# Kernel tuning notes

Hardware: AMD Instinct MI355X
Metric: run time of the kernel (lower is better)

## Reference

```python
import jax, jax.numpy as jnp
import numpy as np

E, H, D = 512, 8, 64          # embed_dim, num_heads, head_dim
MAX_SUM = 128                  # max_summary (embedding table has MAX_SUM+1 rows, row 0 = padding)
SCALE = D ** -0.5


def _linear(x, w, b):
    y = jnp.einsum('...i,oi->...o', x, w)
    return y if b is None else y + b


def setup_inputs() -> dict:
    key = jax.random.key(0)
    ks = jax.random.split(key, 16)
    R, B, S = 2048, 2, 128

    def xav(k, shape, gain=1.0):
        fan_in, fan_out = shape[1], shape[0]
        a = gain * np.sqrt(6.0 / (fan_in + fan_out))
        return jax.random.uniform(k, shape, jnp.float32, -a, a)

    g = 1.0 / np.sqrt(2.0)
    embed_table = jax.random.normal(ks[0], (MAX_SUM + 1, E), jnp.float32) * 0.02
    embed_table = embed_table.at[0].set(0.0)  # padding_idx=0
    return {
        'reg_x': jax.random.normal(ks[1], (R, B, E), jnp.float32),
        'sum_token_ids': jax.random.randint(ks[2], (B, S), 0, MAX_SUM),
        'sum_len': S,
        'reg_len': R,
        'embed_table': embed_table,
        'wq1': xav(ks[3], (E, E), g), 'bq1': jnp.zeros((E,), jnp.float32),
        'wq2': xav(ks[4], (E, E), g), 'bq2': jnp.zeros((E,), jnp.float32),
        'wk': xav(ks[5], (E, E), g),  'bk': jnp.zeros((E,), jnp.float32),
        'wv': xav(ks[6], (E, E), g),  'bv': jnp.zeros((E,), jnp.float32),
        'wo': xav(ks[7], (E, E)),     'bo': jnp.zeros((E,), jnp.float32),
        'sum_gate_w': xav(ks[8], (E, E)),
        'reg_gate_w': xav(ks[9], (E, E)),
        'gate_bias': jax.random.normal(ks[10], (E,), jnp.float32),
    }


def reference(reg_x, sum_token_ids, sum_len, reg_len, embed_table,
              wq1, bq1, wq2, bq2, wk, bk, wv, bv, wo, bo,
              sum_gate_w, reg_gate_w, gate_bias):
    R, B, _ = reg_x.shape
    S = sum_token_ids.shape[1]

    # regular keys/values (shared across all stages)
    reg_k = _linear(reg_x, wk, bk).reshape(R, B, H, D)
    reg_v = _linear(reg_x, wv, bv).reshape(R, B, H, D)

    # ---- stage 1: summary queries (learned summary embeddings) attend to regular tokens
    sum_q = embed_table[sum_token_ids.T].reshape(S, B, H, D)  # [S,B,H,D]
    scores_sr = jnp.einsum('sbhd,rbhd->bhsr', sum_q * SCALE, reg_k)
    w_sr = jax.nn.softmax(scores_sr, axis=-1)
    sum_x2 = jnp.einsum('bhsr,rbhd->sbhd', w_sr, reg_v)       # summary K=V for stage 2

    # ---- stage 2: regular queries attend to summary tokens
    reg_q1 = _linear(reg_x, wq1, bq1).reshape(R, B, H, D)
    scores_rs = jnp.einsum('rbhd,sbhd->bhrs', reg_q1 * SCALE, sum_x2)
    w_rs = jax.nn.softmax(scores_rs, axis=-1)
    sum_output = jnp.einsum('bhrs,sbhd->rbhd', w_rs, sum_x2).reshape(R, B, E)

    # ---- stage 3: regular self-attention
    reg_q2 = _linear(reg_x, wq2, bq2).reshape(R, B, H, D)
    scores_rr = jnp.einsum('qbhd,kbhd->bhqk', reg_q2 * SCALE, reg_k)
    w_rr = jax.nn.softmax(scores_rr, axis=-1)
    reg_output = jnp.einsum('bhqk,kbhd->qbhd', w_rr, reg_v).reshape(R, B, E)

    # ---- gated fusion of summary path and regular path
    gate = jax.nn.sigmoid(_linear(sum_output, sum_gate_w, None)
                          + _linear(reg_output, reg_gate_w, None) + gate_bias)
    attn_output = gate * sum_output + (1.0 - gate) * reg_output
    return _linear(attn_output, wo, bo)
```

## Files before the change

kernel.cpp:

```cpp
#include <hip/hip_runtime.h>
#include <cstdint>
#include <cstddef>

constexpr int R_ = 2048;
constexpr int B_ = 2;
constexpr int S_ = 128;
constexpr int E_ = 512;
constexpr int H_ = 8;
constexpr int D_ = 64;
constexpr int N_ = R_ * B_;
constexpr float SCALE_ = 0.125f;

typedef short bf8_t __attribute__((ext_vector_type(8)));
typedef short bf4_t __attribute__((ext_vector_type(4)));
typedef float f32x4 __attribute__((ext_vector_type(4)));
typedef float f32x16 __attribute__((ext_vector_type(16)));

#define MFMA16(a, b, c) __builtin_amdgcn_mfma_f32_16x16x32_bf16((a), (b), (c), 0, 0, 0)
#define MFMA32(a, b, c) __builtin_amdgcn_mfma_f32_32x32x16_bf16((a), (b), (c), 0, 0, 0)

__device__ __forceinline__ unsigned short f2bf(float f) {
  unsigned u = __builtin_bit_cast(unsigned, f);
  unsigned r = u + 0x7FFFu + ((u >> 16) & 1u);
  return (unsigned short)(r >> 16);
}
__device__ __forceinline__ float bf2f(unsigned short h) {
  unsigned u = ((unsigned)h) << 16;
  return __builtin_bit_cast(float, u);
}

struct WSplitJob { const float* src; unsigned short* dst; };
struct WSplit7 { WSplitJob j[7]; };

__global__ __launch_bounds__(256)
void split_w7_kernel(WSplit7 P)
{
  const WSplitJob jb = P.j[blockIdx.y];
  const int idx = blockIdx.x * 256 + threadIdx.x;
  const int r = idx >> 9, c = idx & 511;
  const float v = jb.src[idx];
  const unsigned short hi = f2bf(v);
  const unsigned short lo = f2bf(v - bf2f(hi));
  unsigned short* d = jb.dst + (size_t)r * 1536 + c;
  d[0] = hi; d[512] = hi; d[1024] = lo;
}

__global__ __launch_bounds__(256)
void split_a_kernel(const float* __restrict__ src, unsigned short* __restrict__ dst)
{
  const int idx = blockIdx.x * 256 + threadIdx.x;
  const int r = idx >> 9, c = idx & 511;
  const float v = src[idx];
  const unsigned short hi = f2bf(v);
  unsigned short* d = dst + ((size_t)r << 10) + c;
  d[0] = hi; d[512] = f2bf(v - bf2f(hi));
}

__global__ __launch_bounds__(256)
void gather_split_kernel(const float* __restrict__ table, const int* __restrict__ ids,
                         unsigned short* __restrict__ qhi, unsigned short* __restrict__ qlo)
{
  const int idx = blockIdx.x * 256 + threadIdx.x;
  const int d = idx & 63;
  const int s = (idx >> 6) & 127;
  const int h = (idx >> 13) & 7;
  const int b = idx >> 16;
  const float v = table[(size_t)ids[b * S_ + s] * E_ + h * 64 + d] * SCALE_;
  const unsigned short hi = f2bf(v);
  qhi[idx] = hi;
  qlo[idx] = f2bf(v - bf2f(hi));
}

struct GemmOut {
  const unsigned short* W;
  const float* bias;
  float scale;
  float* Cf;
  unsigned short* hi;
  unsigned short* lo;
  int mode;
};
struct GemmOuts4 { GemmOut o[4]; };

__global__ __launch_bounds__(256, 4)
void gemm_split_kernel(const unsigned short* __restrict__ A, GemmOuts4 P)
{
  const GemmOut g = P.o[blockIdx.z];
  __shared__ unsigned short As[128][48];
  __shared__ unsigned short Ws[64][48];

  const int tid = threadIdx.x;
  const int w = tid >> 6;
  const int l = tid & 63;
  const int lr = l & 15;
  const int lg = l >> 4;
  const int n0 = blockIdx.x * 128;
  const int o0 = blockIdx.y * 64;

  f32x4 acc[2][4];
#pragma unroll
  for (int m = 0; m < 2; ++m)
#pragma unroll
    for (int n = 0; n < 4; ++n) acc[m][n] = (f32x4){0.f, 0.f, 0.f, 0.f};

  const int ar = tid >> 1;
  const int ac = (tid & 1) * 16;
  const int wr = tid >> 2;
  const int wc = (tid & 3) * 8;

  bf8_t ra0 = *(const bf8_t*)(A + (size_t)(n0 + ar) * 1024 + ac);
  bf8_t ra1 = *(const bf8_t*)(A + (size_t)(n0 + ar) * 1024 + ac + 8);
  bf8_t rw0 = *(const bf8_t*)(g.W + (size_t)(o0 + wr) * 1536 + wc);

  for (int k0 = 0; k0 < 1536; k0 += 32) {
    __syncthreads();
    *(bf8_t*)&As[ar][ac] = ra0;
    *(bf8_t*)&As[ar][ac + 8] = ra1;
    *(bf8_t*)&Ws[wr][wc] = rw0;
    __syncthreads();
    if (k0 + 32 < 1536) {
      const int ak = (k0 + 32) & 1023;
      ra0 = *(const bf8_t*)(A + (size_t)(n0 + ar) * 1024 + ak + ac);
      ra1 = *(const bf8_t*)(A + (size_t)(n0 + ar) * 1024 + ak + ac + 8);
      rw0 = *(const bf8_t*)(g.W + (size_t)(o0 + wr) * 1536 + k0 + 32 + wc);
    }

    bf8_t bvs[4];
#pragma unroll
    for (int n = 0; n < 4; ++n)
      bvs[n] = *(const bf8_t*)&Ws[n * 16 + lr][lg * 8];
#pragma unroll
    for (int m = 0; m < 2; ++m) {
      bf8_t av = *(const bf8_t*)&As[w * 32 + m * 16 + lr][lg * 8];
#pragma unroll
      for (int n = 0; n < 4; ++n)
        acc[m][n] = MFMA16(av, bvs[n], acc[m][n]);
    }
  }

#pragma unroll
  for (int m = 0; m < 2; ++m)
#pragma unroll
    for (int n = 0; n < 4; ++n)
#pragma unroll
      for (int r = 0; r < 4; ++r) {
        const int row = n0 + w * 32 + m * 16 + lg * 4 + r;
        const int col = o0 + n * 16 + lr;
        float v = acc[m][n][r];
        if (g.bias) v += g.bias[col];
        v *= g.scale;
        if (g.mode == 0) {
          g.Cf[((size_t)row << 9) + col] = v;
        } else {
          const int bb = row & 1, rr = row >> 1;
          const int hh = col >> 6, dd = col & 63;
          size_t id;
          if (g.mode == 1) id = (((size_t)(bb * H_ + hh) * R_) + rr) * 64 + dd;
          else             id = (((size_t)(bb * H_ + hh) * 64) + dd) * R_ + rr;
          const unsigned short hv = f2bf(v);
          g.hi[id] = hv;
          g.lo[id] = f2bf(v - bf2f(hv));
        }
      }
}

__global__ __launch_bounds__(256, 4)
void gate_blend_gemm_kernel(const unsigned short* __restrict__ A1,
                            const unsigned short* __restrict__ A2,
                            const unsigned short* __restrict__ W1,
                            const unsigned short* __restrict__ W2,
                            const float* __restrict__ gb,
                            unsigned short* __restrict__ attnP)
{
  __shared__ unsigned short As[128][48];
  __shared__ unsigned short Ws[64][48];

  const int tid = threadIdx.x;
  const int w = tid >> 6;
  const int l = tid & 63;
  const int lr = l & 15;
  const int lg = l >> 4;
  const int n0 = blockIdx.x * 128;
  const int o0 = blockIdx.y * 64;

  f32x4 acc[2][4];
#pragma unroll
  for (int m = 0; m < 2; ++m)
#pragma unroll
    for (int n = 0; n < 4; ++n) acc[m][n] = (f32x4){0.f, 0.f, 0.f, 0.f};

  const int ar = tid >> 1;
  const int ac = (tid & 1) * 16;
  const int wr = tid >> 2;
  const int wc = (tid & 3) * 8;

  auto aP = [&](int kk) {
    const unsigned short* Ax = (kk < 48) ? A1 : A2;
    const int k0 = ((kk < 48) ? kk : kk - 48) * 32;
    return Ax + (size_t)(n0 + ar) * 1024 + (k0 & 1023) + ac;
  };
  auto wP = [&](int kk) {
    const unsigned short* Wx = (kk < 48) ? W1 : W2;
    const int k0 = ((kk < 48) ? kk : kk - 48) * 32;
    return Wx + (size_t)(o0 + wr) * 1536 + k0 + wc;
  };

  bf8_t ra0 = *(const bf8_t*)aP(0);
  bf8_t ra1 = *(const bf8_t*)(aP(0) + 8);
  bf8_t rw0 = *(const bf8_t*)wP(0);

  for (int kk = 0; kk < 96; ++kk) {
    __syncthreads();
    *(bf8_t*)&As[ar][ac] = ra0;
    *(bf8_t*)&As[ar][ac + 8] = ra1;
    *(bf8_t*)&Ws[wr][wc] = rw0;
    __syncthreads();
    if (kk + 1 < 96) {
      ra0 = *(const bf8_t*)aP(kk + 1);
      ra1 = *(const bf8_t*)(aP(kk + 1) + 8);
      rw0 = *(const bf8_t*)wP(kk + 1);
    }

    bf8_t bvs[4];
#pragma unroll
    for (int n = 0; n < 4; ++n)
      bvs[n] = *(const bf8_t*)&Ws[n * 16 + lr][lg * 8];
#pragma unroll
    for (int m = 0; m < 2; ++m) {
      bf8_t av = *(const bf8_t*)&As[w * 32 + m * 16 + lr][lg * 8];
#pragma unroll
      for (int n = 0; n < 4; ++n)
        acc[m][n] = MFMA16(av, bvs[n], acc[m][n]);
    }
  }

#pragma unroll
  for (int m = 0; m < 2; ++m)
#pragma unroll
    for (int n = 0; n < 4; ++n)
#pragma unroll
      for (int r = 0; r < 4; ++r) {
        const int row = n0 + w * 32 + m * 16 + lg * 4 + r;
        const int col = o0 + n * 16 + lr;
        const float t = acc[m][n][r] + gb[col];
        const float gt = 1.0f / (1.0f + __expf(-t));
        const size_t base = (size_t)row << 10;
        const float so = bf2f(A1[base + col]) + bf2f(A1[base + 512 + col]);
        const float ro = bf2f(A2[base + col]) + bf2f(A2[base + 512 + col]);
        const float a = gt * so + (1.0f - gt) * ro;
        const unsigned short hv = f2bf(a);
        attnP[base + col] = hv;
        attnP[base + 512 + col] = f2bf(a - bf2f(hv));
      }
}

__global__ __launch_bounds__(256, 2)
void flash_partial_kernel(const unsigned short* __restrict__ Qhi, const unsigned short* __restrict__ Qlo,
                          const unsigned short* __restrict__ Khi, const unsigned short* __restrict__ Klo,
                          const unsigned short* __restrict__ VtHi, const unsigned short* __restrict__ VtLo,
                          int q_len, int kv_len, int chunk, int zsplit,
                          float* __restrict__ accA, float* __restrict__ accB,
                          float* __restrict__ mlP)
{
  __shared__ unsigned short KsH[32][72];
  __shared__ unsigned short KsL[32][72];
  __shared__ unsigned short VsH[64][40];
  __shared__ unsigned short VsL[64][40];

  const int tid = threadIdx.x;
  const int w = tid >> 6;
  const int l = tid & 63;
  const int lq = l & 31;
  const int hi = l >> 5;
  const int bh = blockIdx.y;
  const int q0 = blockIdx.x * 128;
  const int c = blockIdx.z;
  const int kvbeg = c * chunk;
  const int kvend = kvbeg + chunk;
  const int qrow = q0 + w * 32 + lq;

  bf8_t qh[4], ql[4];
  {
    const size_t qbase = ((size_t)bh * q_len + qrow) * 64;
#pragma unroll
    for (int kd = 0; kd < 4; ++kd) {
      qh[kd] = *(const bf8_t*)(Qhi + qbase + kd * 16 + hi * 8);
      ql[kd] = *(const bf8_t*)(Qlo + qbase + kd * 16 + hi * 8);
    }
  }

  f32x16 acc0 = {0,0,0,0,0,0,0,0,0,0,0,0,0,0,0,0};
  f32x16 acc1 = {0,0,0,0,0,0,0,0,0,0,0,0,0,0,0,0};
  float mrow = -INFINITY;
  float lrow = 0.0f;

  const int sr = tid >> 3;
  const int sc = (tid & 7) * 8;
  const int vd = tid >> 2;
  const int vc = (tid & 3) * 8;

  bf8_t rkh, rkl, rvh, rvl;
  {
    const size_t kb = ((size_t)bh * kv_len + kvbeg + sr) * 64 + sc;
    rkh = *(const bf8_t*)(Khi + kb);
    rkl = *(const bf8_t*)(Klo + kb);
    const size_t vb = ((size_t)bh * 64 + vd) * kv_len + kvbeg + vc;
    rvh = *(const bf8_t*)(VtHi + vb);
    rvl = *(const bf8_t*)(VtLo + vb);
  }

  for (int kv0 = kvbeg; kv0 < kvend; kv0 += 32) {
    __syncthreads();
    *(bf8_t*)&KsH[sr][sc] = rkh;
    *(bf8_t*)&KsL[sr][sc] = rkl;
    *(bf8_t*)&VsH[vd][vc] = rvh;
    *(bf8_t*)&VsL[vd][vc] = rvl;
    __syncthreads();
    if (kv0 + 32 < kvend) {
      const size_t kb = ((size_t)bh * kv_len + kv0 + 32 + sr) * 64 + sc;
      rkh = *(const bf8_t*)(Khi + kb);
      rkl = *(const bf8_t*)(Klo + kb);
      const size_t vb = ((size_t)bh * 64 + vd) * kv_len + kv0 + 32 + vc;
      rvh = *(const bf8_t*)(VtHi + vb);
      rvl = *(const bf8_t*)(VtLo + vb);
    }

    f32x16 s = {0,0,0,0,0,0,0,0,0,0,0,0,0,0,0,0};
#pragma unroll
    for (int kd = 0; kd < 4; ++kd) {
      const bf8_t kfh = *(const bf8_t*)&KsH[lq][kd * 16 + hi * 8];
      const bf8_t kfl = *(const bf8_t*)&KsL[lq][kd * 16 + hi * 8];
      s = MFMA32(kfh, qh[kd], s);
      s = MFMA32(kfh, ql[kd], s);
      s = MFMA32(kfl, qh[kd], s);
    }

    float mx = s[0];
#pragma unroll
    for (int r = 1; r < 16; ++r) mx = fmaxf(mx, s[r]);
    mx = fmaxf(mx, __shfl_xor(mx, 32));
    const float m2 = fmaxf(mrow, mx);
    const float f = __expf(mrow - m2);
    mrow = m2;
    float p[16];
    float ts = 0.f;
#pragma unroll
    for (int r = 0; r < 16; ++r) { p[r] = __expf(s[r] - m2); ts += p[r]; }
    ts += __shfl_xor(ts, 32);
    lrow = lrow * f + ts;
#pragma unroll
    for (int r = 0; r < 16; ++r) { acc0[r] *= f; acc1[r] *= f; }

    bf8_t pah[2], pal[2];
#pragma unroll
    for (int ks = 0; ks < 2; ++ks)
#pragma unroll
      for (int j = 0; j < 8; ++j) {
        const float v = p[ks * 8 + j];
        const unsigned u = __builtin_bit_cast(unsigned, v);
        pah[ks][j] = (short)(u >> 16);
        pal[ks][j] = (short)f2bf(v - __builtin_bit_cast(float, u & 0xFFFF0000u));
      }

#pragma unroll
    for (int ks = 0; ks < 2; ++ks) {
      {
        const bf4_t vh0 = *(const bf4_t*)&VsH[lq][ks * 16 + hi * 4];
        const bf4_t vh1 = *(const bf4_t*)&VsH[lq][ks * 16 + 8 + hi * 4];
        const bf4_t vl0 = *(const bf4_t*)&VsL[lq][ks * 16 + hi * 4];
        const bf4_t vl1 = *(const bf4_t*)&VsL[lq][ks * 16 + 8 + hi * 4];
        const bf8_t vfh = {vh0[0], vh0[1], vh0[2], vh0[3], vh1[0], vh1[1], vh1[2], vh1[3]};
        const bf8_t vfl = {vl0[0], vl0[1], vl0[2], vl0[3], vl1[0], vl1[1], vl1[2], vl1[3]};
        acc0 = MFMA32(vfh, pah[ks], acc0);
        acc0 = MFMA32(vfh, pal[ks], acc0);
        acc0 = MFMA32(vfl, pah[ks], acc0);
      }
      {
        const bf4_t vh0 = *(const bf4_t*)&VsH[32 + lq][ks * 16 + hi * 4];
        const bf4_t vh1 = *(const bf4_t*)&VsH[32 + lq][ks * 16 + 8 + hi * 4];
        const bf4_t vl0 = *(const bf4_t*)&VsL[32 + lq][ks * 16 + hi * 4];
        const bf4_t vl1 = *(const bf4_t*)&VsL[32 + lq][ks * 16 + 8 + hi * 4];
        const bf8_t vfh = {vh0[0], vh0[1], vh0[2], vh0[3], vh1[0], vh1[1], vh1[2], vh1[3]};
        const bf8_t vfl = {vl0[0], vl0[1], vl0[2], vl0[3], vl1[0], vl1[1], vl1[2], vl1[3]};
        acc1 = MFMA32(vfh, pah[ks], acc1);
        acc1 = MFMA32(vfh, pal[ks], acc1);
        acc1 = MFMA32(vfl, pah[ks], acc1);
      }
    }
  }

  const size_t cstride = (size_t)16 * q_len * 64;
  float* accbase = (c < zsplit) ? accA + (size_t)c * cstride
                                : accB + (size_t)(c - zsplit) * cstride;
  float* rowp = accbase + ((size_t)bh * q_len + qrow) * 64;
#pragma unroll
  for (int rg = 0; rg < 4; ++rg) {
    *(float4*)(rowp + rg * 8 + hi * 4) =
        make_float4(acc0[rg * 4 + 0], acc0[rg * 4 + 1], acc0[rg * 4 + 2], acc0[rg * 4 + 3]);
    *(float4*)(rowp + 32 + rg * 8 + hi * 4) =
        make_float4(acc1[rg * 4 + 0], acc1[rg * 4 + 1], acc1[rg * 4 + 2], acc1[rg * 4 + 3]);
  }
  if (l < 32) {
    const int q = q0 + w * 32 + l;
    *(float2*)&mlP[((size_t)(c * 16 + bh) * q_len + q) * 2] = make_float2(mrow, lrow);
  }
}

__global__ __launch_bounds__(256)
void merge_x2_kernel(const float* __restrict__ acc, const float* __restrict__ ml,
                     unsigned short* __restrict__ X2hi, unsigned short* __restrict__ X2lo,
                     unsigned short* __restrict__ X2Thi, unsigned short* __restrict__ X2Tlo)
{
  const int idx = blockIdx.x * 256 + threadIdx.x;
  const int d = idx & 63;
  const int q = (idx >> 6) & 127;
  const int bh = idx >> 13;
  float M = -INFINITY;
#pragma unroll
  for (int c = 0; c < 16; ++c)
    M = fmaxf(M, ml[((size_t)(c * 16 + bh) * 128 + q) * 2]);
  float ls = 0.f, o = 0.f;
#pragma unroll
  for (int c = 0; c < 16; ++c) {
    const size_t mi = ((size_t)(c * 16 + bh) * 128 + q) * 2;
    const float wgt = __expf(ml[mi] - M);
    ls += wgt * ml[mi + 1];
    o += wgt * acc[(size_t)c * 131072 + ((size_t)bh * 128 + q) * 64 + d];
  }
  const float v = o / ls;
  const unsigned short hv = f2bf(v);
  const unsigned short lv = f2bf(v - bf2f(hv));
  X2hi[((size_t)bh * 128 + q) * 64 + d] = hv;
  X2lo[((size_t)bh * 128 + q) * 64 + d] = lv;
  X2Thi[((size_t)bh * 64 + d) * 128 + q] = hv;
  X2Tlo[((size_t)bh * 64 + d) * 128 + q] = lv;
}

__global__ __launch_bounds__(256)
void merge_rows_kernel(const float* __restrict__ accA, const float* __restrict__ accB,
                       const float* __restrict__ ml, int q_len, int qbits, int nc,
                       unsigned short* __restrict__ OutP)
{
  const int idx = blockIdx.x * 256 + threadIdx.x;
  const int d = idx & 63;
  const int q = (idx >> 6) & (q_len - 1);
  const int bh = idx >> (6 + qbits);
  float M = -INFINITY;
  for (int c = 0; c < nc; ++c)
    M = fmaxf(M, ml[((size_t)(c * 16 + bh) * q_len + q) * 2]);
  float ls = 0.f, o = 0.f;
  const size_t aoff = ((size_t)bh * q_len + q) * 64 + d;
  for (int c = 0; c < nc; ++c) {
    const size_t mi = ((size_t)(c * 16 + bh) * q_len + q) * 2;
    const float wgt = __expf(ml[mi] - M);
    ls += wgt * ml[mi + 1];
    const float* a = (c == 0) ? accA : accB;
    o += wgt * a[aoff];
  }
  const float v = o / ls;
  const int b = bh >> 3, h = bh & 7;
  const size_t nrow = (size_t)q * B_ + b;
  const int col = h * 64 + d;
  const unsigned short hv = f2bf(v);
  OutP[nrow * 1024 + col] = hv;
  OutP[nrow * 1024 + 512 + col] = f2bf(v - bf2f(hv));
}

extern "C" void kernel_launch(void* const* d_in, const int* in_sizes, int n_in,
                              void* d_out, int out_size, void* d_ws, size_t ws_size,
                              hipStream_t stream)
{
  const float* reg_x = (const float*)d_in[0];
  const int*   ids   = (const int*)d_in[1];
  const float* table = (const float*)d_in[4];
  const float* wq1 = (const float*)d_in[5];  const float* bq1 = (const float*)d_in[6];
  const float* wq2 = (const float*)d_in[7];  const float* bq2 = (const float*)d_in[8];
  const float* wk  = (const float*)d_in[9];  const float* bk  = (const float*)d_in[10];
  const float* wv  = (const float*)d_in[11]; const float* bv  = (const float*)d_in[12];
  const float* wo  = (const float*)d_in[13]; const float* bo  = (const float*)d_in[14];
  const float* sgw = (const float*)d_in[15];
  const float* rgw = (const float*)d_in[16];
  const float* gb  = (const float*)d_in[17];
  float* out = (float*)d_out;
  char* W = (char*)d_ws;

  const size_t WSLOT  = 1572864;
  const size_t oApair = 0;
  const size_t oW     = 8388608;
  const size_t oKhi   = oW + 7 * WSLOT;
  const size_t oKlo   = oKhi + 4194304;
  const size_t oVtHi  = oKlo + 4194304;
  const size_t oVtLo  = oVtHi + 4194304;
  const size_t oQ1hi  = oVtLo + 4194304;
  const size_t oQ1lo  = oQ1hi + 4194304;
  const size_t oQ2hi  = oQ1lo + 4194304;
  const size_t oQ2lo  = oQ2hi + 4194304;
  const size_t oAcc1  = oQ2lo + 4194304;
  const size_t oSQhi  = oAcc1 + 8388608;
  const size_t oSQlo  = oSQhi + 262144;
  const size_t oX2hi  = oSQlo + 262144;
  const size_t oX2lo  = oX2hi + 262144;
  const size_t oX2Thi = oX2lo + 262144;
  const size_t oX2Tlo = oX2Thi + 262144;
  const size_t oMl    = oX2Tlo + 262144;

  auto U16 = [&](size_t off) { return (unsigned short*)(W + off); };
  auto F32 = [&](size_t off) { return (float*)(W + off); };
  unsigned short* Apair  = U16(oApair);
  unsigned short* Wk3    = U16(oW + 0 * WSLOT);
  unsigned short* Wv3    = U16(oW + 1 * WSLOT);
  unsigned short* Wq13   = U16(oW + 2 * WSLOT);
  unsigned short* Wq23   = U16(oW + 3 * WSLOT);
  unsigned short* Wsg3   = U16(oW + 4 * WSLOT);
  unsigned short* Wrg3   = U16(oW + 5 * WSLOT);
  unsigned short* Wo3    = U16(oW + 6 * WSLOT);
  float*          accS   = F32(oApair);
  float*          accB3  = F32(oAcc1);
  float*          mlP    = F32(oMl);
  unsigned short* sout_p = U16(oQ1hi);
  unsigned short* rout_p = U16(oQ2hi);
  unsigned short* attn_p = U16(oKhi);

  const dim3 blk(256);

  split_a_kernel<<<8192, blk, 0, stream>>>(reg_x, Apair);
  WSplit7 ws7;
  ws7.j[0] = WSplitJob{wk,  Wk3};
  ws7.j[1] = WSplitJob{wv,  Wv3};
  ws7.j[2] = WSplitJob{wq1, Wq13};
  ws7.j[3] = WSplitJob{wq2, Wq23};
  ws7.j[4] = WSplitJob{sgw, Wsg3};
  ws7.j[5] = WSplitJob{rgw, Wrg3};
  ws7.j[6] = WSplitJob{wo,  Wo3};
  split_w7_kernel<<<dim3(1024, 7), blk, 0, stream>>>(ws7);
  gather_split_kernel<<<512, blk, 0, stream>>>(table, ids, U16(oSQhi), U16(oSQlo));

  GemmOuts4 proj;
  proj.o[0].W = Wk3;  proj.o[0].bias = bk;  proj.o[0].scale = 1.0f;   proj.o[0].Cf = nullptr;
  proj.o[0].hi = U16(oKhi);  proj.o[0].lo = U16(oKlo);  proj.o[0].mode = 1;
  proj.o[1].W = Wv3;  proj.o[1].bias = bv;  proj.o[1].scale = 1.0f;   proj.o[1].Cf = nullptr;
  proj.o[1].hi = U16(oVtHi); proj.o[1].lo = U16(oVtLo); proj.o[1].mode = 2;
  proj.o[2].W = Wq13; proj.o[2].bias = bq1; proj.o[2].scale = SCALE_; proj.o[2].Cf = nullptr;
  proj.o[2].hi = U16(oQ1hi); proj.o[2].lo = U16(oQ1lo); proj.o[2].mode = 1;
  proj.o[3].W = Wq23; proj.o[3].bias = bq2; proj.o[3].scale = SCALE_; proj.o[3].Cf = nullptr;
  proj.o[3].hi = U16(oQ2hi); proj.o[3].lo = U16(oQ2lo); proj.o[3].mode = 1;
  gemm_split_kernel<<<dim3(32, 8, 4), blk, 0, stream>>>(Apair, proj);

  flash_partial_kernel<<<dim3(1, 16, 16), blk, 0, stream>>>(
      U16(oSQhi), U16(oSQlo), U16(oKhi), U16(oKlo), U16(oVtHi), U16(oVtLo),
      S_, R_, 128, 16, accS, accS, mlP);
  merge_x2_kernel<<<512, blk, 0, stream>>>(accS, mlP,
      U16(oX2hi), U16(oX2lo), U16(oX2Thi), U16(oX2Tlo));

  flash_partial_kernel<<<dim3(16, 16, 1), blk, 0, stream>>>(
      U16(oQ1hi), U16(oQ1lo), U16(oX2hi), U16(oX2lo), U16(oX2Thi), U16(oX2Tlo),
      R_, S_, 128, 1, accS, accS, mlP);
  merge_rows_kernel<<<8192, blk, 0, stream>>>(accS, accS, mlP, R_, 11, 1, sout_p);

  flash_partial_kernel<<<dim3(16, 16, 2), blk, 0, stream>>>(
      U16(oQ2hi), U16(oQ2lo), U16(oKhi), U16(oKlo), U16(oVtHi), U16(oVtLo),
      R_, R_, 1024, 1, accS, accB3, mlP);
  merge_rows_kernel<<<8192, blk, 0, stream>>>(accS, accB3, mlP, R_, 11, 2, rout_p);

  gate_blend_gemm_kernel<<<dim3(32, 8), blk, 0, stream>>>(
      sout_p, rout_p, Wsg3, Wrg3, gb, attn_p);

  GemmOuts4 gf;
  gf.o[0].W = Wo3; gf.o[0].bias = bo; gf.o[0].scale = 1.0f; gf.o[0].Cf = out;
  gf.o[0].hi = nullptr; gf.o[0].lo = nullptr; gf.o[0].mode = 0;
  gf.o[1] = gf.o[0]; gf.o[2] = gf.o[0]; gf.o[3] = gf.o[0];
  gemm_split_kernel<<<dim3(32, 8, 1), blk, 0, stream>>>(attn_p, gf);
}
```

Before: 244.6 us.

## Fuse split kernels, widen flash KV tile, use exp2 with lazy rescale

```diff
diff --git a/kernel.cpp b/kernel.cpp
--- a/kernel.cpp
+++ b/kernel.cpp
@@ -10,11 +10,13 @@
 constexpr int D_ = 64;
 constexpr int N_ = R_ * B_;
 constexpr float SCALE_ = 0.125f;
+constexpr float LOG2E_ = 1.44269504088896340736f;
+constexpr float SLOG2E_ = SCALE_ * LOG2E_;
 
 typedef short bf8_t __attribute__((ext_vector_type(8)));
-typedef short bf4_t __attribute__((ext_vector_type(4)));
 typedef float f32x4 __attribute__((ext_vector_type(4)));
 typedef float f32x16 __attribute__((ext_vector_type(16)));
+typedef unsigned u32x4 __attribute__((ext_vector_type(4)));
 
 #define MFMA16(a, b, c) __builtin_amdgcn_mfma_f32_16x16x32_bf16((a), (b), (c), 0, 0, 0)
 #define MFMA32(a, b, c) __builtin_amdgcn_mfma_f32_32x32x16_bf16((a), (b), (c), 0, 0, 0)
@@ -28,47 +30,49 @@
   unsigned u = ((unsigned)h) << 16;
   return __builtin_bit_cast(float, u);
 }
+__device__ __forceinline__ int kvperm(int kv) {
+  return (kv & ~15) | (kv & 3) | ((kv & 4) << 1) | ((kv & 8) >> 1);
+}
 
 struct WSplitJob { const float* src; unsigned short* dst; };
 struct WSplit7 { WSplitJob j[7]; };
 
 __global__ __launch_bounds__(256)
-void split_w7_kernel(WSplit7 P)
+void fused_split_kernel(const float* __restrict__ reg_x, unsigned short* __restrict__ Apair,
+                        WSplit7 P, const float* __restrict__ table,
+                        const int* __restrict__ ids,
+                        unsigned short* __restrict__ sqhi, unsigned short* __restrict__ sqlo)
 {
-  const WSplitJob jb = P.j[blockIdx.y];
-  const int idx = blockIdx.x * 256 + threadIdx.x;
-  const int r = idx >> 9, c = idx & 511;
-  const float v = jb.src[idx];
-  const unsigned short hi = f2bf(v);
-  const unsigned short lo = f2bf(v - bf2f(hi));
-  unsigned short* d = jb.dst + (size_t)r * 1536 + c;
-  d[0] = hi; d[512] = hi; d[1024] = lo;
-}
-
-__global__ __launch_bounds__(256)
-void split_a_kernel(const float* __restrict__ src, unsigned short* __restrict__ dst)
-{
-  const int idx = blockIdx.x * 256 + threadIdx.x;
-  const int r = idx >> 9, c = idx & 511;
-  const float v = src[idx];
-  const unsigned short hi = f2bf(v);
-  unsigned short* d = dst + ((size_t)r << 10) + c;
-  d[0] = hi; d[512] = f2bf(v - bf2f(hi));
-}
-
-__global__ __launch_bounds__(256)
-void gather_split_kernel(const float* __restrict__ table, const int* __restrict__ ids,
-                         unsigned short* __restrict__ qhi, unsigned short* __restrict__ qlo)
-{
-  const int idx = blockIdx.x * 256 + threadIdx.x;
-  const int d = idx & 63;
-  const int s = (idx >> 6) & 127;
-  const int h = (idx >> 13) & 7;
-  const int b = idx >> 16;
-  const float v = table[(size_t)ids[b * S_ + s] * E_ + h * 64 + d] * SCALE_;
-  const unsigned short hi = f2bf(v);
-  qhi[idx] = hi;
-  qlo[idx] = f2bf(v - bf2f(hi));
+  const int bx = blockIdx.x;
+  const int tid = threadIdx.x;
+  if (bx < 8192) {
+    const int idx = bx * 256 + tid;
+    const int r = idx >> 9, c = idx & 511;
+    const float v = reg_x[idx];
+    const unsigned short hi = f2bf(v);
+    unsigned short* d = Apair + ((size_t)r << 10) + c;
+    d[0] = hi; d[512] = f2bf(v - bf2f(hi));
+  } else if (bx < 15360) {
+    const int bj = bx - 8192;
+    const WSplitJob jb = P.j[bj >> 10];
+    const int idx = (bj & 1023) * 256 + tid;
+    const int r = idx >> 9, c = idx & 511;
+    const float v = jb.src[idx];
+    const unsigned short hi = f2bf(v);
+    const unsigned short lo = f2bf(v - bf2f(hi));
+    unsigned short* d = jb.dst + (size_t)r * 1536 + c;
+    d[0] = hi; d[512] = hi; d[1024] = lo;
+  } else {
+    const int idx = (bx - 15360) * 256 + tid;
+    const int d = idx & 63;
+    const int s = (idx >> 6) & 127;
+    const int h = (idx >> 13) & 7;
+    const int b = idx >> 16;
+    const float v = table[(size_t)ids[b * S_ + s] * E_ + h * 64 + d] * SLOG2E_;
+    const unsigned short hi = f2bf(v);
+    sqhi[idx] = hi;
+    sqlo[idx] = f2bf(v - bf2f(hi));
+  }
 }
 
 struct GemmOut {
@@ -156,7 +160,7 @@
           const int hh = col >> 6, dd = col & 63;
           size_t id;
           if (g.mode == 1) id = (((size_t)(bb * H_ + hh) * R_) + rr) * 64 + dd;
-          else             id = (((size_t)(bb * H_ + hh) * 64) + dd) * R_ + rr;
+          else             id = (((size_t)(bb * H_ + hh) * 64) + dd) * R_ + kvperm(rr);
           const unsigned short hv = f2bf(v);
           g.hi[id] = hv;
           g.lo[id] = f2bf(v - bf2f(hv));
@@ -258,14 +262,14 @@
 void flash_partial_kernel(const unsigned short* __restrict__ Qhi, const unsigned short* __restrict__ Qlo,
                           const unsigned short* __restrict__ Khi, const unsigned short* __restrict__ Klo,
                           const unsigned short* __restrict__ VtHi, const unsigned short* __restrict__ VtLo,
-                          int q_len, int kv_len, int chunk, int zsplit,
+                          int q_len, int kv_len, int chunk, int zsplit, int out_mode,
                           float* __restrict__ accA, float* __restrict__ accB,
-                          float* __restrict__ mlP)
+                          float* __restrict__ mlP, unsigned short* __restrict__ OutP)
 {
-  __shared__ unsigned short KsH[32][72];
-  __shared__ unsigned short KsL[32][72];
-  __shared__ unsigned short VsH[64][40];
-  __shared__ unsigned short VsL[64][40];
+  __shared__ unsigned short KsH[64][72];
+  __shared__ unsigned short KsL[64][72];
+  __shared__ unsigned short VsH[64][72];
+  __shared__ unsigned short VsL[64][72];
 
   const int tid = threadIdx.x;
   const int w = tid >> 6;
@@ -294,115 +298,156 @@
   float mrow = -INFINITY;
   float lrow = 0.0f;
 
-  const int sr = tid >> 3;
-  const int sc = (tid & 7) * 8;
-  const int vd = tid >> 2;
-  const int vc = (tid & 3) * 8;
-
-  bf8_t rkh, rkl, rvh, rvl;
+  const int sr = tid >> 2;
+  const int sc = (tid & 3) * 16;
+
+  bf8_t rkh[2], rkl[2], rvh[2], rvl[2];
   {
     const size_t kb = ((size_t)bh * kv_len + kvbeg + sr) * 64 + sc;
-    rkh = *(const bf8_t*)(Khi + kb);
-    rkl = *(const bf8_t*)(Klo + kb);
-    const size_t vb = ((size_t)bh * 64 + vd) * kv_len + kvbeg + vc;
-    rvh = *(const bf8_t*)(VtHi + vb);
-    rvl = *(const bf8_t*)(VtLo + vb);
-  }
-
-  for (int kv0 = kvbeg; kv0 < kvend; kv0 += 32) {
+    rkh[0] = *(const bf8_t*)(Khi + kb);  rkh[1] = *(const bf8_t*)(Khi + kb + 8);
+    rkl[0] = *(const bf8_t*)(Klo + kb);  rkl[1] = *(const bf8_t*)(Klo + kb + 8);
+    const size_t vb = ((size_t)bh * 64 + sr) * kv_len + kvbeg + sc;
+    rvh[0] = *(const bf8_t*)(VtHi + vb); rvh[1] = *(const bf8_t*)(VtHi + vb + 8);
+    rvl[0] = *(const bf8_t*)(VtLo + vb); rvl[1] = *(const bf8_t*)(VtLo + vb + 8);
+  }
+
+  for (int kv0 = kvbeg; kv0 < kvend; kv0 += 64) {
     __syncthreads();
-    *(bf8_t*)&KsH[sr][sc] = rkh;
-    *(bf8_t*)&KsL[sr][sc] = rkl;
-    *(bf8_t*)&VsH[vd][vc] = rvh;
-    *(bf8_t*)&VsL[vd][vc] = rvl;
+    *(bf8_t*)&KsH[sr][sc] = rkh[0];  *(bf8_t*)&KsH[sr][sc + 8] = rkh[1];
+    *(bf8_t*)&KsL[sr][sc] = rkl[0];  *(bf8_t*)&KsL[sr][sc + 8] = rkl[1];
+    *(bf8_t*)&VsH[sr][sc] = rvh[0];  *(bf8_t*)&VsH[sr][sc + 8] = rvh[1];
+    *(bf8_t*)&VsL[sr][sc] = rvl[0];  *(bf8_t*)&VsL[sr][sc + 8] = rvl[1];
     __syncthreads();
-    if (kv0 + 32 < kvend) {
-      const size_t kb = ((size_t)bh * kv_len + kv0 + 32 + sr) * 64 + sc;
-      rkh = *(const bf8_t*)(Khi + kb);
-      rkl = *(const bf8_t*)(Klo + kb);
-      const size_t vb = ((size_t)bh * 64 + vd) * kv_len + kv0 + 32 + vc;
-      rvh = *(const bf8_t*)(VtHi + vb);
-      rvl = *(const bf8_t*)(VtLo + vb);
-    }
-
-    f32x16 s = {0,0,0,0,0,0,0,0,0,0,0,0,0,0,0,0};
+    if (kv0 + 64 < kvend) {
+      const size_t kb = ((size_t)bh * kv_len + kv0 + 64 + sr) * 64 + sc;
+      rkh[0] = *(const bf8_t*)(Khi + kb);  rkh[1] = *(const bf8_t*)(Khi + kb + 8);
+      rkl[0] = *(const bf8_t*)(Klo + kb);  rkl[1] = *(const bf8_t*)(Klo + kb + 8);
+      const size_t vb = ((size_t)bh * 64 + sr) * kv_len + kv0 + 64 + sc;
+      rvh[0] = *(const bf8_t*)(VtHi + vb); rvh[1] = *(const bf8_t*)(VtHi + vb + 8);
+      rvl[0] = *(const bf8_t*)(VtLo + vb); rvl[1] = *(const bf8_t*)(VtLo + vb + 8);
+    }
+
+    f32x16 s0 = {0,0,0,0,0,0,0,0,0,0,0,0,0,0,0,0};
+    f32x16 s1 = {0,0,0,0,0,0,0,0,0,0,0,0,0,0,0,0};
+    __builtin_amdgcn_s_setprio(1);
 #pragma unroll
     for (int kd = 0; kd < 4; ++kd) {
-      const bf8_t kfh = *(const bf8_t*)&KsH[lq][kd * 16 + hi * 8];
-      const bf8_t kfl = *(const bf8_t*)&KsL[lq][kd * 16 + hi * 8];
-      s = MFMA32(kfh, qh[kd], s);
-      s = MFMA32(kfh, ql[kd], s);
-      s = MFMA32(kfl, qh[kd], s);
-    }
-
-    float mx = s[0];
-#pragma unroll
-    for (int r = 1; r < 16; ++r) mx = fmaxf(mx, s[r]);
+      const bf8_t kfh0 = *(const bf8_t*)&KsH[lq][kd * 16 + hi * 8];
+      const bf8_t kfl0 = *(const bf8_t*)&KsL[lq][kd * 16 + hi * 8];
+      s0 = MFMA32(kfh0, qh[kd], s0);
+      s0 = MFMA32(kfh0, ql[kd], s0);
+      s0 = MFMA32(kfl0, qh[kd], s0);
+      const bf8_t kfh1 = *(const bf8_t*)&KsH[32 + lq][kd * 16 + hi * 8];
+      const bf8_t kfl1 = *(const bf8_t*)&KsL[32 + lq][kd * 16 + hi * 8];
+      s1 = MFMA32(kfh1, qh[kd], s1);
+      s1 = MFMA32(kfh1, ql[kd], s1);
+      s1 = MFMA32(kfl1, qh[kd], s1);
+    }
+    __builtin_amdgcn_s_setprio(0);
+
+    float mx = fmaxf(s0[0], s1[0]);
+#pragma unroll
+    for (int r = 1; r < 16; ++r) mx = fmaxf(mx, fmaxf(s0[r], s1[r]));
     mx = fmaxf(mx, __shfl_xor(mx, 32));
-    const float m2 = fmaxf(mrow, mx);
-    const float f = __expf(mrow - m2);
-    mrow = m2;
-    float p[16];
+    if (mx > mrow + 8.0f) {
+      const float f = exp2f(mrow - mx);
+      mrow = mx;
+      lrow *= f;
+#pragma unroll
+      for (int r = 0; r < 16; ++r) { acc0[r] *= f; acc1[r] *= f; }
+    }
     float ts = 0.f;
 #pragma unroll
-    for (int r = 0; r < 16; ++r) { p[r] = __expf(s[r] - m2); ts += p[r]; }
+    for (int r = 0; r < 16; ++r) { s0[r] = exp2f(s0[r] - mrow); ts += s0[r]; }
+#pragma unroll
+    for (int r = 0; r < 16; ++r) { s1[r] = exp2f(s1[r] - mrow); ts += s1[r]; }
     ts += __shfl_xor(ts, 32);
-    lrow = lrow * f + ts;
-#pragma unroll
-    for (int r = 0; r < 16; ++r) { acc0[r] *= f; acc1[r] *= f; }
-
-    bf8_t pah[2], pal[2];
-#pragma unroll
-    for (int ks = 0; ks < 2; ++ks)
-#pragma unroll
-      for (int j = 0; j < 8; ++j) {
-        const float v = p[ks * 8 + j];
-        const unsigned u = __builtin_bit_cast(unsigned, v);
-        pah[ks][j] = (short)(u >> 16);
-        pal[ks][j] = (short)f2bf(v - __builtin_bit_cast(float, u & 0xFFFF0000u));
+    lrow += ts;
+
+    bf8_t pah[4], pal[4];
+#pragma unroll
+    for (int n = 0; n < 2; ++n)
+#pragma unroll
+      for (int ks = 0; ks < 2; ++ks) {
+        u32x4 hp, lp;
+#pragma unroll
+        for (int p2 = 0; p2 < 4; ++p2) {
+          const float a = n ? s1[ks * 8 + p2 * 2]     : s0[ks * 8 + p2 * 2];
+          const float b = n ? s1[ks * 8 + p2 * 2 + 1] : s0[ks * 8 + p2 * 2 + 1];
+          const unsigned ua = __builtin_bit_cast(unsigned, a);
+          const unsigned ub = __builtin_bit_cast(unsigned, b);
+          hp[p2] = (ua >> 16) | (ub & 0xFFFF0000u);
+          const float la = a - __builtin_bit_cast(float, ua & 0xFFFF0000u);
+          const float lb = b - __builtin_bit_cast(float, ub & 0xFFFF0000u);
+          lp[p2] = (__builtin_bit_cast(unsigned, la) >> 16) |
+                   (__builtin_bit_cast(unsigned, lb) & 0xFFFF0000u);
+        }
+        pah[n * 2 + ks] = __builtin_bit_cast(bf8_t, hp);
+        pal[n * 2 + ks] = __builtin_bit_cast(bf8_t, lp);
       }
 
-#pragma unroll
-    for (int ks = 0; ks < 2; ++ks) {
-      {
-        const bf4_t vh0 = *(const bf4_t*)&VsH[lq][ks * 16 + hi * 4];
-        const bf4_t vh1 = *(const bf4_t*)&VsH[lq][ks * 16 + 8 + hi * 4];
-        const bf4_t vl0 = *(const bf4_t*)&VsL[lq][ks * 16 + hi * 4];
-        const bf4_t vl1 = *(const bf4_t*)&VsL[lq][ks * 16 + 8 + hi * 4];
-        const bf8_t vfh = {vh0[0], vh0[1], vh0[2], vh0[3], vh1[0], vh1[1], vh1[2], vh1[3]};
-        const bf8_t vfl = {vl0[0], vl0[1], vl0[2], vl0[3], vl1[0], vl1[1], vl1[2], vl1[3]};
-        acc0 = MFMA32(vfh, pah[ks], acc0);
-        acc0 = MFMA32(vfh, pal[ks], acc0);
-        acc0 = MFMA32(vfl, pah[ks], acc0);
+    __builtin_amdgcn_s_setprio(1);
+#pragma unroll
+    for (int n = 0; n < 2; ++n)
+#pragma unroll
+      for (int ks = 0; ks < 2; ++ks) {
+        const int vcol = n * 32 + ks * 16 + hi * 8;
+        const bf8_t ph = pah[n * 2 + ks];
+        const bf8_t pl = pal[n * 2 + ks];
+        {
+          const bf8_t vfh = *(const bf8_t*)&VsH[lq][vcol];
+          const bf8_t vfl = *(const bf8_t*)&VsL[lq][vcol];
+          acc0 = MFMA32(vfh, ph, acc0);
+          acc0 = MFMA32(vfh, pl, acc0);
+          acc0 = MFMA32(vfl, ph, acc0);
+        }
+        {
+          const bf8_t vfh = *(const bf8_t*)&VsH[32 + lq][vcol];
+          const bf8_t vfl = *(const bf8_t*)&VsL[32 + lq][vcol];
+          acc1 = MFMA32(vfh, ph, acc1);
+          acc1 = MFMA32(vfh, pl, acc1);
+          acc1 = MFMA32(vfl, ph, acc1);
+        }
       }
-      {
-        const bf4_t vh0 = *(const bf4_t*)&VsH[32 + lq][ks * 16 + hi * 4];
-        const bf4_t vh1 = *(const bf4_t*)&VsH[32 + lq][ks * 16 + 8 + hi * 4];
-        const bf4_t vl0 = *(const bf4_t*)&VsL[32 + lq][ks * 16 + hi * 4];
-        const bf4_t vl1 = *(const bf4_t*)&VsL[32 + lq][ks * 16 + 8 + hi * 4];
-        const bf8_t vfh = {vh0[0], vh0[1], vh0[2], vh0[3], vh1[0], vh1[1], vh1[2], vh1[3]};
-        const bf8_t vfl = {vl0[0], vl0[1], vl0[2], vl0[3], vl1[0], vl1[1], vl1[2], vl1[3]};
-        acc1 = MFMA32(vfh, pah[ks], acc1);
-        acc1 = MFMA32(vfh, pal[ks], acc1);
-        acc1 = MFMA32(vfl, pah[ks], acc1);
+    __builtin_amdgcn_s_setprio(0);
+  }
+
+  if (out_mode == 0) {
+    const size_t cstride = (size_t)16 * q_len * 64;
+    float* accbase = (c < zsplit) ? accA + (size_t)c * cstride
+                                  : accB + (size_t)(c - zsplit) * cstride;
+    float* rowp = accbase + ((size_t)bh * q_len + qrow) * 64;
+#pragma unroll
+    for (int rg = 0; rg < 4; ++rg) {
+      *(float4*)(rowp + rg * 8 + hi * 4) =
+          make_float4(acc0[rg * 4 + 0], acc0[rg * 4 + 1], acc0[rg * 4 + 2], acc0[rg * 4 + 3]);
+      *(float4*)(rowp + 32 + rg * 8 + hi * 4) =
+          make_float4(acc1[rg * 4 + 0], acc1[rg * 4 + 1], acc1[rg * 4 + 2], acc1[rg * 4 + 3]);
+    }
+    if (l < 32) {
+      const int q = q0 + w * 32 + l;
+      *(float2*)&mlP[((size_t)(c * 16 + bh) * q_len + q) * 2] = make_float2(mrow, lrow);
+    }
+  } else {
+    const float inv = 1.0f / lrow;
+    const int b = bh >> 3, h = bh & 7;
+    const size_t base = ((size_t)qrow * B_ + b) << 10;
+#pragma unroll
+    for (int hd = 0; hd < 2; ++hd)
+#pragma unroll
+      for (int rg = 0; rg < 4; ++rg) {
+        const int col = h * 64 + hd * 32 + rg * 8 + hi * 4;
+        ushort4 hv4, lv4;
+#pragma unroll
+        for (int i = 0; i < 4; ++i) {
+          const float v = (hd ? acc1[rg * 4 + i] : acc0[rg * 4 + i]) * inv;
+          const unsigned short hv = f2bf(v);
+          ((unsigned short*)&hv4)[i] = hv;
+          ((unsigned short*)&lv4)[i] = f2bf(v - bf2f(hv));
+        }
+        *(ushort4*)&OutP[base + col] = hv4;
+        *(ushort4*)&OutP[base + 512 + col] = lv4;
       }
-    }
-  }
-
-  const size_t cstride = (size_t)16 * q_len * 64;
-  float* accbase = (c < zsplit) ? accA + (size_t)c * cstride
-                                : accB + (size_t)(c - zsplit) * cstride;
-  float* rowp = accbase + ((size_t)bh * q_len + qrow) * 64;
-#pragma unroll
-  for (int rg = 0; rg < 4; ++rg) {
-    *(float4*)(rowp + rg * 8 + hi * 4) =
-        make_float4(acc0[rg * 4 + 0], acc0[rg * 4 + 1], acc0[rg * 4 + 2], acc0[rg * 4 + 3]);
-    *(float4*)(rowp + 32 + rg * 8 + hi * 4) =
-        make_float4(acc1[rg * 4 + 0], acc1[rg * 4 + 1], acc1[rg * 4 + 2], acc1[rg * 4 + 3]);
-  }
-  if (l < 32) {
-    const int q = q0 + w * 32 + l;
-    *(float2*)&mlP[((size_t)(c * 16 + bh) * q_len + q) * 2] = make_float2(mrow, lrow);
   }
 }
 
@@ -423,7 +468,7 @@
 #pragma unroll
   for (int c = 0; c < 16; ++c) {
     const size_t mi = ((size_t)(c * 16 + bh) * 128 + q) * 2;
-    const float wgt = __expf(ml[mi] - M);
+    const float wgt = exp2f(ml[mi] - M);
     ls += wgt * ml[mi + 1];
     o += wgt * acc[(size_t)c * 131072 + ((size_t)bh * 128 + q) * 64 + d];
   }
@@ -432,32 +477,27 @@
   const unsigned short lv = f2bf(v - bf2f(hv));
   X2hi[((size_t)bh * 128 + q) * 64 + d] = hv;
   X2lo[((size_t)bh * 128 + q) * 64 + d] = lv;
-  X2Thi[((size_t)bh * 64 + d) * 128 + q] = hv;
-  X2Tlo[((size_t)bh * 64 + d) * 128 + q] = lv;
+  const int qp = kvperm(q);
+  X2Thi[((size_t)bh * 64 + d) * 128 + qp] = hv;
+  X2Tlo[((size_t)bh * 64 + d) * 128 + qp] = lv;
 }
 
 __global__ __launch_bounds__(256)
 void merge_rows_kernel(const float* __restrict__ accA, const float* __restrict__ accB,
-                       const float* __restrict__ ml, int q_len, int qbits, int nc,
-                       unsigned short* __restrict__ OutP)
+                       const float* __restrict__ ml, unsigned short* __restrict__ OutP)
 {
   const int idx = blockIdx.x * 256 + threadIdx.x;
   const int d = idx & 63;
-  const int q = (idx >> 6) & (q_len - 1);
-  const int bh = idx >> (6 + qbits);
-  float M = -INFINITY;
-  for (int c = 0; c < nc; ++c)
-    M = fmaxf(M, ml[((size_t)(c * 16 + bh) * q_len + q) * 2]);
-  float ls = 0.f, o = 0.f;
-  const size_t aoff = ((size_t)bh * q_len + q) * 64 + d;
-  for (int c = 0; c < nc; ++c) {
-    const size_t mi = ((size_t)(c * 16 + bh) * q_len + q) * 2;
-    const float wgt = __expf(ml[mi] - M);
-    ls += wgt * ml[mi + 1];
-    const float* a = (c == 0) ? accA : accB;
-    o += wgt * a[aoff];
-  }
-  const float v = o / ls;
+  const int q = (idx >> 6) & 2047;
+  const int bh = idx >> 17;
+  const size_t mi0 = ((size_t)bh * 2048 + q) * 2;
+  const size_t mi1 = ((size_t)(16 + bh) * 2048 + q) * 2;
+  const float m0 = ml[mi0], m1 = ml[mi1];
+  const float M = fmaxf(m0, m1);
+  const float w0 = exp2f(m0 - M), w1 = exp2f(m1 - M);
+  const float ls = w0 * ml[mi0 + 1] + w1 * ml[mi1 + 1];
+  const size_t aoff = ((size_t)bh * 2048 + q) * 64 + d;
+  const float v = (w0 * accA[aoff] + w1 * accB[aoff]) / ls;
   const int b = bh >> 3, h = bh & 7;
   const size_t nrow = (size_t)q * B_ + b;
   const int col = h * 64 + d;
@@ -523,7 +563,6 @@
 
   const dim3 blk(256);
 
-  split_a_kernel<<<8192, blk, 0, stream>>>(reg_x, Apair);
   WSplit7 ws7;
   ws7.j[0] = WSplitJob{wk,  Wk3};
   ws7.j[1] = WSplitJob{wv,  Wv3};
@@ -532,35 +571,34 @@
   ws7.j[4] = WSplitJob{sgw, Wsg3};
   ws7.j[5] = WSplitJob{rgw, Wrg3};
   ws7.j[6] = WSplitJob{wo,  Wo3};
-  split_w7_kernel<<<dim3(1024, 7), blk, 0, stream>>>(ws7);
-  gather_split_kernel<<<512, blk, 0, stream>>>(table, ids, U16(oSQhi), U16(oSQlo));
+  fused_split_kernel<<<15872, blk, 0, stream>>>(reg_x, Apair, ws7, table, ids,
+                                                U16(oSQhi), U16(oSQlo));
 
   GemmOuts4 proj;
-  proj.o[0].W = Wk3;  proj.o[0].bias = bk;  proj.o[0].scale = 1.0f;   proj.o[0].Cf = nullptr;
+  proj.o[0].W = Wk3;  proj.o[0].bias = bk;  proj.o[0].scale = 1.0f;    proj.o[0].Cf = nullptr;
   proj.o[0].hi = U16(oKhi);  proj.o[0].lo = U16(oKlo);  proj.o[0].mode = 1;
-  proj.o[1].W = Wv3;  proj.o[1].bias = bv;  proj.o[1].scale = 1.0f;   proj.o[1].Cf = nullptr;
+  proj.o[1].W = Wv3;  proj.o[1].bias = bv;  proj.o[1].scale = 1.0f;    proj.o[1].Cf = nullptr;
   proj.o[1].hi = U16(oVtHi); proj.o[1].lo = U16(oVtLo); proj.o[1].mode = 2;
-  proj.o[2].W = Wq13; proj.o[2].bias = bq1; proj.o[2].scale = SCALE_; proj.o[2].Cf = nullptr;
+  proj.o[2].W = Wq13; proj.o[2].bias = bq1; proj.o[2].scale = SLOG2E_; proj.o[2].Cf = nullptr;
   proj.o[2].hi = U16(oQ1hi); proj.o[2].lo = U16(oQ1lo); proj.o[2].mode = 1;
-  proj.o[3].W = Wq23; proj.o[3].bias = bq2; proj.o[3].scale = SCALE_; proj.o[3].Cf = nullptr;
+  proj.o[3].W = Wq23; proj.o[3].bias = bq2; proj.o[3].scale = SLOG2E_; proj.o[3].Cf = nullptr;
   proj.o[3].hi = U16(oQ2hi); proj.o[3].lo = U16(oQ2lo); proj.o[3].mode = 1;
   gemm_split_kernel<<<dim3(32, 8, 4), blk, 0, stream>>>(Apair, proj);
 
   flash_partial_kernel<<<dim3(1, 16, 16), blk, 0, stream>>>(
       U16(oSQhi), U16(oSQlo), U16(oKhi), U16(oKlo), U16(oVtHi), U16(oVtLo),
-      S_, R_, 128, 16, accS, accS, mlP);
+      S_, R_, 128, 16, 0, accS, accS, mlP, nullptr);
   merge_x2_kernel<<<512, blk, 0, stream>>>(accS, mlP,
       U16(oX2hi), U16(oX2lo), U16(oX2Thi), U16(oX2Tlo));
 
   flash_partial_kernel<<<dim3(16, 16, 1), blk, 0, stream>>>(
       U16(oQ1hi), U16(oQ1lo), U16(oX2hi), U16(oX2lo), U16(oX2Thi), U16(oX2Tlo),
-      R_, S_, 128, 1, accS, accS, mlP);
-  merge_rows_kernel<<<8192, blk, 0, stream>>>(accS, accS, mlP, R_, 11, 1, sout_p);
+      R_, S_, 128, 1, 1, accS, accS, mlP, sout_p);
 
   flash_partial_kernel<<<dim3(16, 16, 2), blk, 0, stream>>>(
       U16(oQ2hi), U16(oQ2lo), U16(oKhi), U16(oKlo), U16(oVtHi), U16(oVtLo),
-      R_, R_, 1024, 1, accS, accB3, mlP);
-  merge_rows_kernel<<<8192, blk, 0, stream>>>(accS, accB3, mlP, R_, 11, 2, rout_p);
+      R_, R_, 1024, 1, 0, accS, accB3, mlP, nullptr);
+  merge_rows_kernel<<<8192, blk, 0, stream>>>(accS, accB3, mlP, rout_p);
 
   gate_blend_gemm_kernel<<<dim3(32, 8), blk, 0, stream>>>(
       sout_p, rout_p, Wsg3, Wrg3, gb, attn_p);
```

Result: faster. 230.5 us (-5.8%).
